# Optimization experiments

Measured on AMD Instinct MI355X. Metric: run time of the kernel, lower is better.

The kernel has to match this reference:

```python
import jax, jax.numpy as jnp
import numpy as np

N, E, IN, HID, OUT = 50000, 800000, 256, 256, 64
HEADS, DH = 4, 64  # GAT: hidden//4 per head, concat=False -> mean over heads
EPS = 1e-5


def _gcn(x, W, b, src, dst):
    # PyG GCNConv: h = xW; add self-loops; sym-normalized scatter-add; + bias
    n = x.shape[0]
    h = x @ W
    deg = jnp.zeros((n,), x.dtype).at[dst].add(1.0) + 1.0  # +1 for self-loop
    dinv = jax.lax.rsqrt(deg)
    norm = dinv[src] * dinv[dst]                      # [E]
    out = jax.ops.segment_sum(h[src] * norm[:, None], dst, num_segments=n)
    out = out + h * (dinv * dinv)[:, None]            # self-loop term
    return out + b


def _gat(x, W, a_s, a_d, b, src, dst):
    # PyG GATConv(heads=HEADS, concat=False): per-edge attention softmax over
    # incoming edges (incl. self-loop), LeakyReLU(0.2) logits, mean over heads.
    n = x.shape[0]
    h = (x @ W).reshape(n, HEADS, DH)
    al_s = jnp.einsum('nhd,hd->nh', h, a_s)           # [N,H]
    al_d = jnp.einsum('nhd,hd->nh', h, a_d)
    e = jax.nn.leaky_relu(al_s[src] + al_d[dst], 0.2)  # [E,H]
    e_self = jax.nn.leaky_relu(al_s + al_d, 0.2)       # [N,H]
    m = jnp.maximum(jax.ops.segment_max(e, dst, num_segments=n), e_self)
    ee = jnp.exp(e - m[dst])
    es = jnp.exp(e_self - m)
    denom = jax.ops.segment_sum(ee, dst, num_segments=n) + es        # [N,H]
    numer = jax.ops.segment_sum(ee[:, :, None] * h[src], dst, num_segments=n) + es[:, :, None] * h
    return (numer / denom[:, :, None]).mean(axis=1) + b


def _bn(x, g, b):
    # BatchNorm1d over node dim, batch statistics (training-mode math)
    mu = x.mean(axis=0)
    var = x.var(axis=0)
    return g * (x - mu) * jax.lax.rsqrt(var + EPS) + b


def setup_inputs() -> dict:
    key = jax.random.key(0)
    ks = jax.random.split(key, 12)
    s = lambda d: 1.0 / np.sqrt(d)
    inp = {
        'x': jax.random.normal(ks[0], (N, IN), jnp.float32),
        'edge_index': jax.random.randint(ks[1], (2, E), 0, N, jnp.int64),
        'W1': jax.random.normal(ks[2], (IN, HID), jnp.float32) * s(IN),
        'b1': jnp.zeros((HID,), jnp.float32),
        'g1': jnp.ones((HID,), jnp.float32),
        'be1': jnp.zeros((HID,), jnp.float32),
        'Wg': jax.random.normal(ks[3], (HID, HEADS * DH), jnp.float32) * s(HID),
        'a_src': jax.random.normal(ks[4], (HEADS, DH), jnp.float32) * s(DH),
        'a_dst': jax.random.normal(ks[5], (HEADS, DH), jnp.float32) * s(DH),
        'bg': jnp.zeros((DH,), jnp.float32),
        'g2': jnp.ones((DH,), jnp.float32),
        'be2': jnp.zeros((DH,), jnp.float32),
        'W3': jax.random.normal(ks[6], (64, 16), jnp.float32) * s(64),
        'b3': jnp.zeros((16,), jnp.float32),
        'g3': jnp.ones((16,), jnp.float32),
        'be3': jnp.zeros((16,), jnp.float32),
        'W4': jax.random.normal(ks[7], (16, OUT), jnp.float32) * s(16),
        'b4': jnp.zeros((OUT,), jnp.float32),
        'r1W': jax.random.normal(ks[8], (IN, HID), jnp.float32) * s(IN),
        'r1b': jnp.zeros((HID,), jnp.float32),
        'r2W': jax.random.normal(ks[9], (HID, 64), jnp.float32) * s(HID),
        'r2b': jnp.zeros((64,), jnp.float32),
        'r3W': jax.random.normal(ks[10], (64, 16), jnp.float32) * s(64),
        'r3b': jnp.zeros((16,), jnp.float32),
        'pW': jax.random.normal(ks[11], (OUT, OUT), jnp.float32) * s(OUT),
        'pb': jnp.zeros((OUT,), jnp.float32),
    }
    return inp


def reference(x, edge_index, W1, b1, g1, be1, Wg, a_src, a_dst, bg, g2, be2,
              W3, b3, g3, be3, W4, b4, r1W, r1b, r2W, r2b, r3W, r3b, pW, pb):
    src, dst = edge_index[0], edge_index[1]
    slope = 0.01  # F.leaky_relu default; dropout is identity at inference
    x0 = x
    h = _gcn(x0, W1, b1, src, dst)
    h = jax.nn.leaky_relu(_bn(h, g1, be1), slope)
    h = h + (x0 @ r1W + r1b)
    x2 = h
    h = _gat(x2, Wg, a_src, a_dst, bg, src, dst)
    h = jax.nn.leaky_relu(_bn(h, g2, be2), slope)
    h = h + (x2 @ r2W + r2b)
    x3 = h
    h = _gcn(x3, W3, b3, src, dst)
    h = jax.nn.leaky_relu(_bn(h, g3, be3), slope)
    h = h + (x3 @ r3W + r3b)
    h = _gcn(h, W4, b4, src, dst)
    return h @ pW + pb
```

## Files before the change

kernel.cpp:

```cpp
#include <hip/hip_runtime.h>

typedef unsigned short u16;
typedef unsigned int   u32;

__device__ __forceinline__ float b2f(u16 h){ return __uint_as_float(((u32)h)<<16); }
__device__ __forceinline__ u16 f2b(float f){
  u32 u = __float_as_uint(f);
  u32 r = (u + 0x7fffu + ((u>>16)&1u)) >> 16;
  return (u16)r;
}
__device__ __forceinline__ float leaky(float x, float s){ return x >= 0.f ? x : s*x; }

typedef __bf16 bf16x8 __attribute__((ext_vector_type(8)));
typedef float  f32x4  __attribute__((ext_vector_type(4)));

__device__ __forceinline__ float ldval(const u16* p){ return b2f(*p); }
__device__ __forceinline__ float ldval(const float* p){ return *p; }

__device__ __forceinline__ void load8(const u16* p, u16* h){ *(uint4*)h = *(const uint4*)p; }
__device__ __forceinline__ void load8(const float* p, u16* h){
  float4 a = *(const float4*)p; float4 b = *(const float4*)(p+4);
  h[0]=f2b(a.x); h[1]=f2b(a.y); h[2]=f2b(a.z); h[3]=f2b(a.w);
  h[4]=f2b(b.x); h[5]=f2b(b.y); h[6]=f2b(b.z); h[7]=f2b(b.w);
}

__global__ void k_detect(const u32* __restrict__ w, int E, u32* __restrict__ flag){
  u32 acc = 0;
  for (int i = blockIdx.x*256 + threadIdx.x; i < E; i += 256*gridDim.x)
    acc |= w[2*i + 1];
  __shared__ u32 s[256];
  s[threadIdx.x] = acc; __syncthreads();
  for (int o=128;o>0;o>>=1){ if (threadIdx.x<o) s[threadIdx.x] |= s[threadIdx.x+o]; __syncthreads(); }
  if (threadIdx.x==0 && s[0]) atomicOr(flag, 1u);
}

__device__ __forceinline__ void edge_sd(const int* __restrict__ ei, int E, int e, u32 is32,
                                        int& s, int& d){
  if (is32){ s = ei[e];   d = ei[E + e]; }
  else     { s = ei[2*e]; d = ei[2*E + 2*e]; }
}

__global__ void k_hist(const int* __restrict__ ei, int E, int nN,
                       const u32* __restrict__ flag, int* __restrict__ cnt){
  int e = blockIdx.x*256 + threadIdx.x;
  if (e < E){
    int s,d; edge_sd(ei, E, e, *flag, s, d);
    if ((u32)s < (u32)nN && (u32)d < (u32)nN) atomicAdd(&cnt[d], 1);
  }
}

__global__ void k_scan_a(const int* __restrict__ cnt, int n, int* __restrict__ bsum){
  __shared__ int s[256];
  int base = blockIdx.x*1024, t = threadIdx.x, sum = 0;
  for (int j=0;j<4;j++){ int i = base + t*4 + j; if (i<n) sum += cnt[i]; }
  s[t] = sum; __syncthreads();
  for (int off=128; off>0; off>>=1){ if (t<off) s[t]+=s[t+off]; __syncthreads(); }
  if (t==0) bsum[blockIdx.x] = s[0];
}

__global__ void k_scan_b(int* bsum, int nb){
  if (threadIdx.x==0 && blockIdx.x==0){
    int acc = 0;
    for (int i=0;i<nb;i++){ int v = bsum[i]; bsum[i] = acc; acc += v; }
  }
}

__global__ void k_scan_c(const int* __restrict__ cnt, const int* __restrict__ bsum,
                         int n, int* __restrict__ offs){
  __shared__ int s[256];
  int base = blockIdx.x*1024, t = threadIdx.x;
  int v[4]; int sum=0;
  for (int j=0;j<4;j++){ int i=base+t*4+j; v[j] = (i<n)?cnt[i]:0; sum += v[j]; }
  s[t]=sum; __syncthreads();
  for (int off=1; off<256; off<<=1){
    int add = (t>=off)? s[t-off] : 0;
    __syncthreads();
    s[t] += add;
    __syncthreads();
  }
  int excl = (t ? s[t-1] : 0) + bsum[blockIdx.x];
  for (int j=0;j<4;j++){
    int i = base+t*4+j;
    if (i<n){ offs[i] = excl; excl += v[j]; if (i==n-1) offs[n] = excl; }
  }
}

__global__ void k_dinv2(const int* __restrict__ offs, int n, float* __restrict__ dinv){
  int i = blockIdx.x*256+threadIdx.x;
  if (i<n) dinv[i] = rsqrtf((float)(offs[i+1]-offs[i]) + 1.0f);
}

__global__ void k_scatter(const int* __restrict__ ei, int E, int nN,
                          const u32* __restrict__ flag, const int* __restrict__ offs,
                          int* __restrict__ cursor, int* __restrict__ csr){
  int e = blockIdx.x*256+threadIdx.x;
  if (e<E){
    int s,d; edge_sd(ei, E, e, *flag, s, d);
    if ((u32)s < (u32)nN && (u32)d < (u32)nN){
      int pos = offs[d] + atomicAdd(&cursor[d], 1);
      csr[pos] = s;
    }
  }
}

__global__ void k_transpose(const float* __restrict__ in, u16* __restrict__ out, int K, int M){
  int i = blockIdx.x*256 + threadIdx.x;
  if (i < K*M){ int k = i / M, m = i % M; out[m*K + k] = f2b(in[i]); }
}

__global__ void k_asdt(const float* __restrict__ a_s, const float* __restrict__ a_d,
                       float* __restrict__ asi, float* __restrict__ adi){
  int i = threadIdx.x;
  int h = i>>6, c = i&63;
  asi[c*4+h] = a_s[i];
  adi[c*4+h] = a_d[i];
}

template<typename AT>
__global__ __launch_bounds__(256) void k_gemm64(
  const AT* __restrict__ A0, const AT* __restrict__ A1,
  const AT* __restrict__ A2, const AT* __restrict__ A3,
  int rsA, const u16* __restrict__ Bt, const float* __restrict__ bias,
  u16* __restrict__ out, int nRows)
{
  alignas(16) __shared__ u16 Al[64*264];
  const int t = threadIdx.x;
  const int r0 = blockIdx.x*64;
  for (int it=0; it<8; ++it){
    int c = t + it*256;
    int row = c>>5, seg = c&31;
    int gr = r0+row;
    u16 hv[8] = {0,0,0,0,0,0,0,0};
    if (gr < nRows){
      const AT* p = (seg<8)?A0 : (seg<16)?A1 : (seg<24)?A2 : A3;
      load8(p + (size_t)gr*rsA + (seg&7)*8, hv);
    }
    *(uint4*)&Al[row*264 + seg*8] = *(uint4*)hv;
  }
  const int lane=t&63, wid=t>>6, quad=lane>>4, l15=lane&15;
  __syncthreads();
  const int col = wid*16 + l15;
  const u16* Bp = Bt + (size_t)col*256 + quad*8;
  bf16x8 b[8];
  #pragma unroll
  for (int ks=0;ks<8;++ks) b[ks] = *(const bf16x8*)(Bp + ks*32);
  f32x4 acc[4] = {{0.f,0.f,0.f,0.f},{0.f,0.f,0.f,0.f},{0.f,0.f,0.f,0.f},{0.f,0.f,0.f,0.f}};
  #pragma unroll
  for (int rt=0; rt<4; ++rt){
    const int abase = (rt*16 + l15)*264 + quad*8;
    #pragma unroll
    for (int ks=0;ks<8;++ks){
      bf16x8 av = *(const bf16x8*)&Al[abase + ks*32];
      acc[rt] = __builtin_amdgcn_mfma_f32_16x16x32_bf16(av, b[ks], acc[rt], 0,0,0);
    }
  }
  __syncthreads();
  float bv = bias ? bias[col] : 0.f;
  #pragma unroll
  for (int rt=0; rt<4; ++rt){
    #pragma unroll
    for (int reg=0;reg<4;++reg)
      Al[(rt*16 + quad*4 + reg)*264 + col] = f2b(acc[rt][reg]+bv);
  }
  __syncthreads();
  #pragma unroll
  for (int it=0; it<2; ++it){
    int idx = it*256 + t;
    int row = idx>>3, cu = idx&7;
    if (r0+row < nRows)
      *(uint4*)(out + (size_t)(r0+row)*64 + cu*8) = *(const uint4*)&Al[row*264 + cu*8];
  }
}

template<typename AT, bool PERM, bool EW, bool DOT, bool RS>
__global__ __launch_bounds__(512) void k_gemm256(
  const AT* __restrict__ A0, const AT* __restrict__ A1,
  const AT* __restrict__ A2, const AT* __restrict__ A3,
  int rsA, const u16* __restrict__ Bt, const float* __restrict__ bias,
  const u16* __restrict__ agg, const float* __restrict__ bnp,
  const float* __restrict__ asi, const float* __restrict__ adi,
  float* __restrict__ als, float* __restrict__ ald,
  const float* __restrict__ rowscale,
  u16* __restrict__ out, int nRows)
{
  alignas(16) __shared__ u16 Al[64*264];
  const int t = threadIdx.x;
  const int r0 = blockIdx.x*64;
  for (int it=0; it<4; ++it){
    int c = t + it*512;
    int row = c>>5, seg = c&31;
    int gr = r0+row;
    u16 hv[8] = {0,0,0,0,0,0,0,0};
    if (gr < nRows){
      const AT* p = (seg<8)?A0 : (seg<16)?A1 : (seg<24)?A2 : A3;
      load8(p + (size_t)gr*rsA + (seg&7)*8, hv);
    }
    *(uint4*)&Al[row*264 + seg*8] = *(uint4*)hv;
  }
  const int lane=t&63, wid=t>>6, quad=lane>>4, l15=lane&15;
  __syncthreads();
  f32x4 acc[2][4];
  #pragma unroll
  for (int ct=0; ct<2; ++ct)
    #pragma unroll
    for (int rt=0; rt<4; ++rt) acc[ct][rt] = {0.f,0.f,0.f,0.f};
  #pragma unroll
  for (int ct=0; ct<2; ++ct){
    const u16* Bp = Bt + (size_t)(wid*32 + ct*16 + l15)*256 + quad*8;
    #pragma unroll
    for (int ks=0;ks<8;++ks){
      bf16x8 b = *(const bf16x8*)(Bp + ks*32);
      #pragma unroll
      for (int rt=0; rt<4; ++rt){
        bf16x8 av = *(const bf16x8*)&Al[(rt*16 + l15)*264 + quad*8 + ks*32];
        acc[ct][rt] = __builtin_amdgcn_mfma_f32_16x16x32_bf16(av, b, acc[ct][rt], 0,0,0);
      }
    }
  }
  __syncthreads();
  #pragma unroll
  for (int ct=0; ct<2; ++ct){
    int col = wid*32 + ct*16 + l15;
    float bv = bias ? bias[col] : 0.f;
    int oc = PERM ? ((col&63)*4 + (col>>6)) : col;
    #pragma unroll
    for (int rt=0; rt<4; ++rt){
      #pragma unroll
      for (int reg=0;reg<4;++reg){
        float v = acc[ct][rt][reg] + bv;
        if constexpr (RS){
          int r = r0 + rt*16 + quad*4 + reg;
          v *= (r < nRows) ? rowscale[r] : 1.f;
        }
        Al[(rt*16 + quad*4 + reg)*264 + oc] = f2b(v);
      }
    }
  }
  __syncthreads();
  if constexpr (DOT){
    int row = t>>3, q = t&7;
    int nd = r0 + row;
    if (nd < nRows){
      float s0=0.f,s1=0.f,s2=0.f,s3=0.f,d0=0.f,d1=0.f,d2=0.f,d3=0.f;
      const u16* ar = &Al[row*264 + q*32];
      const float* as = asi + q*32;
      const float* ad = adi + q*32;
      #pragma unroll 4
      for (int k=0;k<32;k+=4){
        uint2 wv = *(const uint2*)&ar[k];
        float v0=b2f((u16)(wv.x&0xffff)), v1=b2f((u16)(wv.x>>16));
        float v2=b2f((u16)(wv.y&0xffff)), v3=b2f((u16)(wv.y>>16));
        s0 += v0*as[k];   d0 += v0*ad[k];
        s1 += v1*as[k+1]; d1 += v1*ad[k+1];
        s2 += v2*as[k+2]; d2 += v2*ad[k+2];
        s3 += v3*as[k+3]; d3 += v3*ad[k+3];
      }
      s0 += __shfl_xor(s0,1,64); s0 += __shfl_xor(s0,2,64); s0 += __shfl_xor(s0,4,64);
      s1 += __shfl_xor(s1,1,64); s1 += __shfl_xor(s1,2,64); s1 += __shfl_xor(s1,4,64);
      s2 += __shfl_xor(s2,1,64); s2 += __shfl_xor(s2,2,64); s2 += __shfl_xor(s2,4,64);
      s3 += __shfl_xor(s3,1,64); s3 += __shfl_xor(s3,2,64); s3 += __shfl_xor(s3,4,64);
      d0 += __shfl_xor(d0,1,64); d0 += __shfl_xor(d0,2,64); d0 += __shfl_xor(d0,4,64);
      d1 += __shfl_xor(d1,1,64); d1 += __shfl_xor(d1,2,64); d1 += __shfl_xor(d1,4,64);
      d2 += __shfl_xor(d2,1,64); d2 += __shfl_xor(d2,2,64); d2 += __shfl_xor(d2,4,64);
      d3 += __shfl_xor(d3,1,64); d3 += __shfl_xor(d3,2,64); d3 += __shfl_xor(d3,4,64);
      if (q==0){
        float4 sv = {s0,s1,s2,s3}; float4 dv = {d0,d1,d2,d3};
        ((float4*)als)[nd] = sv;
        ((float4*)ald)[nd] = dv;
      }
    }
  }
  #pragma unroll
  for (int it=0; it<4; ++it){
    int idx = it*512 + t;
    int row = idx>>5, cu = idx&31;
    int r = r0+row;
    if (r < nRows){
      if constexpr (EW){
        uint4 hv = *(const uint4*)&Al[row*264 + cu*8];
        uint4 av = *(const uint4*)(agg + (size_t)r*256 + cu*8);
        const u16* hp = (const u16*)&hv; const u16* ap = (const u16*)&av;
        uint4 ov; u16* op = (u16*)&ov;
        #pragma unroll
        for (int j=0;j<8;++j){
          int c = cu*8+j;
          float v = b2f(ap[j])*bnp[c] + bnp[256+c];
          op[j] = f2b(leaky(v, 0.01f) + b2f(hp[j]));
        }
        *(uint4*)(out + (size_t)r*256 + cu*8) = ov;
      } else {
        *(uint4*)(out + (size_t)r*256 + cu*8) = *(const uint4*)&Al[row*264 + cu*8];
      }
    }
  }
}

__global__ void k_gather64(const u16* __restrict__ h, const int* __restrict__ offs,
                           const int* __restrict__ csr, const float* __restrict__ dinv,
                           const float* __restrict__ bias, int n, u16* __restrict__ out){
  int nd = blockIdx.x*4 + (threadIdx.x>>6);
  if (nd>=n) return;
  int lane = threadIdx.x&63;
  float dn = dinv[nd];
  float acc = dn*b2f(h[(size_t)nd*64+lane]);
  int e = offs[nd], end = offs[nd+1];
  for (; e+4<=end; e+=4){
    int s0=csr[e], s1=csr[e+1], s2=csr[e+2], s3=csr[e+3];
    float w0=dinv[s0], w1=dinv[s1], w2=dinv[s2], w3=dinv[s3];
    float p0=b2f(h[(size_t)s0*64+lane]);
    float p1=b2f(h[(size_t)s1*64+lane]);
    float p2=b2f(h[(size_t)s2*64+lane]);
    float p3=b2f(h[(size_t)s3*64+lane]);
    acc += w0*p0 + w1*p1 + w2*p2 + w3*p3;
  }
  for (; e<end; ++e){
    int s=csr[e];
    acc += dinv[s]*b2f(h[(size_t)s*64+lane]);
  }
  out[(size_t)nd*64+lane] = f2b(dn*acc + bias[lane]);
}

__global__ void k_gather256(const u16* __restrict__ h, const int* __restrict__ offs,
                            const int* __restrict__ csr, const float* __restrict__ dinv,
                            const float* __restrict__ bias, int n, u16* __restrict__ out){
  int nd = blockIdx.x*4 + (threadIdx.x>>6);
  if (nd>=n) return;
  int lane = threadIdx.x&63;
  const uint2* H = (const uint2*)h;
  float dn = dinv[nd];
  uint2 pv = H[(size_t)nd*64 + lane];
  float a0=b2f(pv.x&0xffff), a1=b2f(pv.x>>16);
  float a2=b2f(pv.y&0xffff), a3=b2f(pv.y>>16);
  int e=offs[nd], end=offs[nd+1];
  for (; e+4<=end; e+=4){
    int s0=csr[e], s1=csr[e+1], s2=csr[e+2], s3=csr[e+3];
    uint2 q0=H[(size_t)s0*64+lane], q1=H[(size_t)s1*64+lane];
    uint2 q2=H[(size_t)s2*64+lane], q3=H[(size_t)s3*64+lane];
    a0 += b2f(q0.x&0xffff) + b2f(q1.x&0xffff) + b2f(q2.x&0xffff) + b2f(q3.x&0xffff);
    a1 += b2f(q0.x>>16)    + b2f(q1.x>>16)    + b2f(q2.x>>16)    + b2f(q3.x>>16);
    a2 += b2f(q0.y&0xffff) + b2f(q1.y&0xffff) + b2f(q2.y&0xffff) + b2f(q3.y&0xffff);
    a3 += b2f(q0.y>>16)    + b2f(q1.y>>16)    + b2f(q2.y>>16)    + b2f(q3.y>>16);
  }
  for (; e<end; ++e){
    int s=csr[e];
    uint2 q=H[(size_t)s*64+lane];
    a0 += b2f(q.x&0xffff); a1 += b2f(q.x>>16);
    a2 += b2f(q.y&0xffff); a3 += b2f(q.y>>16);
  }
  float4 bv = *(const float4*)(bias + lane*4);
  uint2 o;
  o.x = (u32)f2b(a0*dn + bv.x) | ((u32)f2b(a1*dn + bv.y)<<16);
  o.y = (u32)f2b(a2*dn + bv.z) | ((u32)f2b(a3*dn + bv.w)<<16);
  ((uint2*)out)[(size_t)nd*64 + lane] = o;
}

template<typename T, int C>
__global__ __launch_bounds__(256) void k_stats_part(const T* __restrict__ x, int n,
                                                    float* __restrict__ part){
  constexpr int VE = 16/sizeof(T);
  constexpr int G  = C/VE;
  constexpr int R  = 256/G;
  int t = threadIdx.x;
  int g = t % G, sub = t / G;
  int rpb = (n + gridDim.x - 1) / gridDim.x;
  int base = blockIdx.x * rpb;
  int lim  = min(base + rpb, n);
  float s[VE], s2[VE];
  #pragma unroll
  for (int j=0;j<VE;j++){ s[j]=0.f; s2[j]=0.f; }
  #pragma unroll 4
  for (int r = base + sub; r < lim; r += R){
    const T* p = x + (size_t)r*C + g*VE;
    if constexpr (sizeof(T)==2){
      uint4 v = *(const uint4*)p;
      u32 wq[4] = {v.x, v.y, v.z, v.w};
      #pragma unroll
      for (int q=0;q<4;q++){
        float lo = __uint_as_float(wq[q]<<16);
        float hi = __uint_as_float(wq[q]&0xffff0000u);
        s[2*q]  += lo; s2[2*q]  += lo*lo;
        s[2*q+1]+= hi; s2[2*q+1]+= hi*hi;
      }
    } else {
      float4 v = *(const float4*)p;
      float a[4] = {v.x, v.y, v.z, v.w};
      #pragma unroll
      for (int q=0;q<4;q++){ s[q]+=a[q]; s2[q]+=a[q]*a[q]; }
    }
  }
  __shared__ float red[VE][256];
  #pragma unroll
  for (int j=0;j<VE;j++) red[j][t] = s[j];
  __syncthreads();
  for (int off=R/2; off>0; off>>=1){
    if (sub < off){
      #pragma unroll
      for (int j=0;j<VE;j++) red[j][t] += red[j][t + off*G];
    }
    __syncthreads();
  }
  if (t < G){
    #pragma unroll
    for (int j=0;j<VE;j++) part[blockIdx.x*2*C + t*VE + j] = red[j][t];
  }
  __syncthreads();
  #pragma unroll
  for (int j=0;j<VE;j++) red[j][t] = s2[j];
  __syncthreads();
  for (int off=R/2; off>0; off>>=1){
    if (sub < off){
      #pragma unroll
      for (int j=0;j<VE;j++) red[j][t] += red[j][t + off*G];
    }
    __syncthreads();
  }
  if (t < G){
    #pragma unroll
    for (int j=0;j<VE;j++) part[blockIdx.x*2*C + C + t*VE + j] = red[j][t];
  }
}

template<int C>
__global__ __launch_bounds__(256) void k_bnfin3(const float* __restrict__ part, int B,
                         const float* __restrict__ g, const float* __restrict__ be,
                         float n, float* __restrict__ bnp){
  constexpr int CPB = (C < 32) ? C : 32;
  constexpr int TPC = 256 / CPB;
  int t = threadIdx.x;
  int lc = t % CPB, sub = t / CPB;
  int c = blockIdx.x*CPB + lc;
  float s=0.f, s2=0.f;
  for (int b = sub; b < B; b += TPC){
    s  += part[(size_t)b*2*C + c];
    s2 += part[(size_t)b*2*C + C + c];
  }
  __shared__ float ls[256], lq[256];
  ls[t]=s; lq[t]=s2; __syncthreads();
  for (int off=TPC/2; off>0; off>>=1){
    if (sub < off){ ls[t]+=ls[t+off*CPB]; lq[t]+=lq[t+off*CPB]; }
    __syncthreads();
  }
  if (sub==0){
    float mu = ls[t]/n;
    float var = fmaxf(lq[t]/n - mu*mu, 0.f);
    float sc = g[c] * rsqrtf(var + 1e-5f);
    bnp[c] = sc;
    bnp[C+c] = be[c] - mu*sc;
  }
}

__global__ void k_ew_b16b16(const u16* __restrict__ agg, const u16* __restrict__ res,
                            const float* __restrict__ bnp, int C, int total, u16* __restrict__ out){
  int i = blockIdx.x*256+threadIdx.x;
  if (i < total){
    int c = i & (C-1);
    float v = b2f(agg[i])*bnp[c] + bnp[C+c];
    out[i] = f2b(leaky(v, 0.01f) + b2f(res[i]));
  }
}

__global__ void k_ew_f32f32(const float* __restrict__ agg, const float* __restrict__ res,
                            const float* __restrict__ bnp, int C, int total, float* __restrict__ out){
  int i = blockIdx.x*256+threadIdx.x;
  if (i < total){
    int c = i & (C-1);
    float v = agg[i]*bnp[c] + bnp[C+c];
    out[i] = leaky(v, 0.01f) + res[i];
  }
}

__global__ void k_dot64(const u16* __restrict__ h2t, const float* __restrict__ asg,
                        const float* __restrict__ adg, int head, int n,
                        float* __restrict__ als, float* __restrict__ ald){
  int nd = blockIdx.x*4 + (threadIdx.x>>6);
  if (nd>=n) return;
  int lane = threadIdx.x&63;
  float p = b2f(h2t[(size_t)nd*64+lane]);
  float ss = p*asg[lane];
  float sd = p*adg[lane];
  for (int m=1;m<64;m<<=1){ ss += __shfl_xor(ss,m,64); sd += __shfl_xor(sd,m,64); }
  if (lane==0){ als[nd*4+head]=ss; ald[nd*4+head]=sd; }
}

__global__ void k_gat_head(const u16* __restrict__ h2t, const int* __restrict__ offs,
                           const int* __restrict__ csr, const float* __restrict__ als,
                           const float* __restrict__ ald, const float* __restrict__ bg,
                           int head, int n, u16* __restrict__ O2){
  int nd = blockIdx.x*4 + (threadIdx.x>>6);
  if (nd>=n) return;
  int lane = threadIdx.x&63;
  float aldn = ald[nd*4+head];
  float m = leaky(als[nd*4+head] + aldn, 0.2f);
  float denom = 1.f;
  float acc = b2f(h2t[(size_t)nd*64+lane]);
  int e = offs[nd], end = offs[nd+1];
  for (; e+4<=end; e+=4){
    int s0=csr[e], s1=csr[e+1], s2=csr[e+2], s3=csr[e+3];
    float l0=als[s0*4+head], l1=als[s1*4+head], l2=als[s2*4+head], l3=als[s3*4+head];
    float p0=b2f(h2t[(size_t)s0*64+lane]);
    float p1=b2f(h2t[(size_t)s1*64+lane]);
    float p2=b2f(h2t[(size_t)s2*64+lane]);
    float p3=b2f(h2t[(size_t)s3*64+lane]);
    float g0=leaky(l0+aldn,0.2f), g1=leaky(l1+aldn,0.2f);
    float g2=leaky(l2+aldn,0.2f), g3=leaky(l3+aldn,0.2f);
    float mc = fmaxf(fmaxf(g0,g1), fmaxf(g2,g3));
    float mn = fmaxf(m, mc);
    float sc = __expf(m - mn);
    float w0 = __expf(g0-mn), w1 = __expf(g1-mn), w2 = __expf(g2-mn), w3 = __expf(g3-mn);
    denom = denom*sc + (w0+w1+w2+w3);
    acc   = acc*sc   + (w0*p0 + w1*p1 + w2*p2 + w3*p3);
    m = mn;
  }
  for (; e<end; ++e){
    int s = csr[e];
    float g = leaky(als[s*4+head]+aldn, 0.2f);
    float p = b2f(h2t[(size_t)s*64+lane]);
    float mn = fmaxf(m, g);
    float sc = __expf(m - mn);
    float w = __expf(g - mn);
    denom = denom*sc + w;
    acc   = acc*sc   + w*p;
    m = mn;
  }
  float v = 0.25f * acc / fmaxf(denom, 1e-20f);
  size_t oi = (size_t)nd*64+lane;
  if (head==0) O2[oi] = f2b(v + bg[lane]);
  else         O2[oi] = f2b(b2f(O2[oi]) + v);
}

__global__ void k_gat_all(const u16* __restrict__ h2i, const int* __restrict__ offs,
                          const int* __restrict__ csr, const float* __restrict__ als,
                          const float* __restrict__ ald, const float* __restrict__ bg,
                          int n, u16* __restrict__ O2){
  alignas(16) __shared__ float shm[4][80];
  int wv = threadIdx.x>>6;
  int nd = blockIdx.x*4 + wv;
  if (nd>=n) return;
  int lane = threadIdx.x&63;
  int eg = lane>>2, hh = lane&3;
  float4 alv = ((const float4*)als)[nd];
  float4 adv = ((const float4*)ald)[nd];
  float adh = (hh&2) ? ((hh&1)?adv.w:adv.z) : ((hh&1)?adv.y:adv.x);
  float alh = (hh&2) ? ((hh&1)?alv.w:alv.z) : ((hh&1)?alv.y:alv.x);
  float gsh = leaky(alh+adh, 0.2f);
  int beg=offs[nd], end=offs[nd+1];
  float m = gsh;
  for (int e=beg+eg; e<end; e+=16){
    int s = csr[e];
    m = fmaxf(m, leaky(als[s*4+hh]+adh, 0.2f));
  }
  #pragma unroll
  for (int off=4; off<64; off<<=1) m = fmaxf(m, __shfl_xor(m, off, 64));
  float wsh = __expf(gsh - m);
  if (eg==0) shm[wv][4+hh] = wsh;
  float4 ws4 = *(const float4*)&shm[wv][4];
  uint2 pv = ((const uint2*)h2i)[(size_t)nd*64+lane];
  float a0 = ws4.x*__uint_as_float(pv.x<<16);
  float a1 = ws4.y*__uint_as_float(pv.x&0xffff0000u);
  float a2 = ws4.z*__uint_as_float(pv.y<<16);
  float a3 = ws4.w*__uint_as_float(pv.y&0xffff0000u);
  float dpart = 0.f;
  const uint2* H = (const uint2*)h2i;
  for (int e0=beg; e0<end; e0+=16){
    int e = e0+eg;
    int sA = 0; float wE = 0.f;
    if (e<end){
      sA = csr[e];
      wE = __expf(leaky(als[sA*4+hh]+adh, 0.2f) - m);
    }
    dpart += wE;
    shm[wv][8+lane] = wE;
    int cnt = min(16, end-e0);
    int k=0;
    for (; k+4<=cnt; k+=4){
      int sa=__shfl(sA,(k  )*4,64), sb=__shfl(sA,(k+1)*4,64);
      int sc=__shfl(sA,(k+2)*4,64), sd=__shfl(sA,(k+3)*4,64);
      float4 wa=*(const float4*)&shm[wv][8+(k  )*4];
      float4 wb=*(const float4*)&shm[wv][8+(k+1)*4];
      float4 wc=*(const float4*)&shm[wv][8+(k+2)*4];
      float4 wd=*(const float4*)&shm[wv][8+(k+3)*4];
      uint2 qa=H[(size_t)sa*64+lane], qb=H[(size_t)sb*64+lane];
      uint2 qc=H[(size_t)sc*64+lane], qd=H[(size_t)sd*64+lane];
      a0 += wa.x*__uint_as_float(qa.x<<16) + wb.x*__uint_as_float(qb.x<<16)
          + wc.x*__uint_as_float(qc.x<<16) + wd.x*__uint_as_float(qd.x<<16);
      a1 += wa.y*__uint_as_float(qa.x&0xffff0000u) + wb.y*__uint_as_float(qb.x&0xffff0000u)
          + wc.y*__uint_as_float(qc.x&0xffff0000u) + wd.y*__uint_as_float(qd.x&0xffff0000u);
      a2 += wa.z*__uint_as_float(qa.y<<16) + wb.z*__uint_as_float(qb.y<<16)
          + wc.z*__uint_as_float(qc.y<<16) + wd.z*__uint_as_float(qd.y<<16);
      a3 += wa.w*__uint_as_float(qa.y&0xffff0000u) + wb.w*__uint_as_float(qb.y&0xffff0000u)
          + wc.w*__uint_as_float(qc.y&0xffff0000u) + wd.w*__uint_as_float(qd.y&0xffff0000u);
    }
    for (; k<cnt; ++k){
      int s = __shfl(sA, k*4, 64);
      float4 w4 = *(const float4*)&shm[wv][8+k*4];
      uint2 q = H[(size_t)s*64+lane];
      a0 += w4.x*__uint_as_float(q.x<<16);
      a1 += w4.y*__uint_as_float(q.x&0xffff0000u);
      a2 += w4.z*__uint_as_float(q.y<<16);
      a3 += w4.w*__uint_as_float(q.y&0xffff0000u);
    }
  }
  #pragma unroll
  for (int off=4; off<64; off<<=1) dpart += __shfl_xor(dpart, off, 64);
  float dh = dpart + wsh;
  if (eg==0) shm[wv][hh] = dh;
  float4 d4 = *(const float4*)&shm[wv][0];
  float v = 0.25f*(a0/d4.x + a1/d4.y + a2/d4.z + a3/d4.w);
  O2[(size_t)nd*64+lane] = f2b(v + bg[lane]);
}

__global__ void k_gcn_agg16(const float* __restrict__ h, const int* __restrict__ offs,
                            const int* __restrict__ csr, const float* __restrict__ dinv,
                            const float* __restrict__ bias, float* __restrict__ out, int n){
  int t = threadIdx.x;
  int nd = blockIdx.x*16 + (t>>4);
  if (nd>=n) return;
  int c = t&15;
  float dn = dinv[nd];
  float acc = h[(size_t)nd*16+c];
  int e=offs[nd], end=offs[nd+1];
  for (; e+4<=end; e+=4){
    int s0=csr[e], s1=csr[e+1], s2=csr[e+2], s3=csr[e+3];
    acc += h[(size_t)s0*16+c] + h[(size_t)s1*16+c]
         + h[(size_t)s2*16+c] + h[(size_t)s3*16+c];
  }
  for (; e<end; ++e){
    int s = csr[e];
    acc += h[(size_t)s*16+c];
  }
  out[(size_t)nd*16+c] = dn*acc + bias[c];
}

__global__ void k_gcn_agg64f(const float* __restrict__ h, const int* __restrict__ offs,
                             const int* __restrict__ csr, const float* __restrict__ dinv,
                             const float* __restrict__ bias, float* __restrict__ out, int n){
  int nd = blockIdx.x*4 + (threadIdx.x>>6);
  if (nd>=n) return;
  int lane = threadIdx.x&63;
  float dn = dinv[nd];
  float acc = h[(size_t)nd*64+lane];
  int e=offs[nd], end=offs[nd+1];
  for (; e+4<=end; e+=4){
    int s0=csr[e], s1=csr[e+1], s2=csr[e+2], s3=csr[e+3];
    acc += h[(size_t)s0*64+lane] + h[(size_t)s1*64+lane]
         + h[(size_t)s2*64+lane] + h[(size_t)s3*64+lane];
  }
  for (; e<end; ++e){
    int s=csr[e];
    acc += h[(size_t)s*64+lane];
  }
  out[(size_t)nd*64+lane] = dn*acc + bias[lane];
}

__global__ void k_gemm64_16x2(const u16* __restrict__ x, const float* __restrict__ W1_,
                              const float* __restrict__ W2_, const float* __restrict__ b2_,
                              const float* __restrict__ dinv,
                              int n, float* __restrict__ o1, float* __restrict__ o2){
  __shared__ float w1[64*16], w2[64*16];
  int t = threadIdx.x;
  for (int i=t; i<1024; i+=256){ w1[i]=W1_[i]; w2[i]=W2_[i]; }
  __syncthreads();
  int nd = blockIdx.x*8 + (t>>5);
  if (nd>=n) return;
  int j = t & 31;
  const u16* xr = x + (size_t)nd*64;
  if (j<16){
    float s=0.f;
    #pragma unroll 8
    for (int k=0;k<64;k++) s += b2f(xr[k])*w1[k*16+j];
    o1[(size_t)nd*16+j]=s*dinv[nd];
  } else {
    int jj=j-16;
    float s = b2_[jj];
    #pragma unroll 8
    for (int k=0;k<64;k++) s += b2f(xr[k])*w2[k*16+jj];
    o2[(size_t)nd*16+jj]=s;
  }
}

__global__ void k_gemm16_64(const float* __restrict__ x, const float* __restrict__ W,
                            const float* __restrict__ dinv,
                            int n, float* __restrict__ o){
  __shared__ float w[16*64];
  int t = threadIdx.x;
  for (int i=t;i<1024;i+=256) w[i]=W[i];
  __syncthreads();
  int nd = blockIdx.x*4 + (t>>6);
  if (nd>=n) return;
  int j = t&63;
  const float* xr = x + (size_t)nd*16;
  float s=0.f;
  #pragma unroll
  for (int k=0;k<16;k++) s += xr[k]*w[k*64+j];
  o[(size_t)nd*64+j]=s*dinv[nd];
}

__global__ void k_final(const float* __restrict__ x, const float* __restrict__ W,
                        const float* __restrict__ b, int n, float* __restrict__ out){
  __shared__ float w[64*64];
  int t=threadIdx.x;
  for (int i=t;i<4096;i+=256) w[i]=W[i];
  __syncthreads();
  int nd = blockIdx.x*4 + (t>>6);
  if (nd>=n) return;
  int j=t&63;
  const float* xr = x + (size_t)nd*64;
  float s=b[j];
  #pragma unroll 8
  for (int k=0;k<64;k++) s += xr[k]*w[k*64+j];
  out[(size_t)nd*64+j]=s;
}

extern "C" void kernel_launch(void* const* d_in, const int* in_sizes, int n_in,
                              void* d_out, int out_size, void* d_ws, size_t ws_size,
                              hipStream_t stream) {
  const float* x   = (const float*)d_in[0];
  const int*   ei  = (const int*)d_in[1];
  const float* W1  = (const float*)d_in[2];
  const float* b1  = (const float*)d_in[3];
  const float* g1  = (const float*)d_in[4];
  const float* be1 = (const float*)d_in[5];
  const float* Wg  = (const float*)d_in[6];
  const float* a_s = (const float*)d_in[7];
  const float* a_d = (const float*)d_in[8];
  const float* bg  = (const float*)d_in[9];
  const float* g2  = (const float*)d_in[10];
  const float* be2 = (const float*)d_in[11];
  const float* W3  = (const float*)d_in[12];
  const float* b3  = (const float*)d_in[13];
  const float* g3  = (const float*)d_in[14];
  const float* be3 = (const float*)d_in[15];
  const float* W4  = (const float*)d_in[16];
  const float* b4  = (const float*)d_in[17];
  const float* r1W = (const float*)d_in[18];
  const float* r1b = (const float*)d_in[19];
  const float* r2W = (const float*)d_in[20];
  const float* r2b = (const float*)d_in[21];
  const float* r3W = (const float*)d_in[22];
  const float* r3b = (const float*)d_in[23];
  const float* pW  = (const float*)d_in[24];
  const float* pb  = (const float*)d_in[25];

  const int N = in_sizes[0] / 256;
  const int E = in_sizes[1] / 2;

  char* w = (char*)d_ws;
  auto alloc = [&](size_t b)->void*{ void* p=(void*)w; w += (b+255)&~(size_t)255; return p; };
  u32*   flag   = (u32*)  alloc(4);
  float* part   = (float*)alloc(256*512*4);
  float* bnp1   = (float*)alloc(512*4);
  float* bnp2   = (float*)alloc(128*4);
  float* bnp3   = (float*)alloc(32*4);
  int*   bsum   = (int*)  alloc(256*4);
  int*   cur    = (int*)  alloc((size_t)N*4);
  int*   offs   = (int*)  alloc((size_t)(N+1)*4);
  float* dinv   = (float*)alloc((size_t)N*4);
  int*   csr    = (int*)  alloc((size_t)E*4);
  float* als    = (float*)alloc((size_t)N*16);
  float* ald    = (float*)alloc((size_t)N*16);
  float* asi    = (float*)alloc(256*4);
  float* adi    = (float*)alloc(256*4);
  u16*   W1t    = (u16*)  alloc(65536*2);
  u16*   r1Wt   = (u16*)  alloc(65536*2);
  u16*   Wgt    = (u16*)  alloc(65536*2);
  u16*   r2Wt   = (u16*)  alloc(16384*2);

  auto cdiv = [](int a, int b){ return (a+b-1)/b; };
  const int nb1024 = cdiv(N, 1024);
  const int statsGrid = 256;
  const int gemmGrid = cdiv(N,64);
  const int nodeGrid = cdiv(N,4);

  hipMemsetAsync(flag,   0, 4, stream);
  hipMemsetAsync(cur,    0, (size_t)N*4, stream);

  k_detect<<<64,256,0,stream>>>((const u32*)ei, E, flag);

  k_transpose<<<cdiv(65536,256),256,0,stream>>>(W1,  W1t,  256,256);
  k_transpose<<<cdiv(65536,256),256,0,stream>>>(r1W, r1Wt, 256,256);
  k_transpose<<<cdiv(65536,256),256,0,stream>>>(Wg,  Wgt,  256,256);
  k_transpose<<<cdiv(16384,256),256,0,stream>>>(r2W, r2Wt, 256,64);
  k_asdt<<<1,256,0,stream>>>(a_s, a_d, asi, adi);

  k_hist  <<<cdiv(E,256),256,0,stream>>>(ei, E, N, flag, cur);
  k_scan_a<<<nb1024,256,0,stream>>>(cur, N, bsum);
  k_scan_b<<<1,64,0,stream>>>(bsum, nb1024);
  k_scan_c<<<nb1024,256,0,stream>>>(cur, bsum, N, offs);
  k_dinv2 <<<cdiv(N,256),256,0,stream>>>(offs, N, dinv);
  hipMemsetAsync(cur, 0, (size_t)N*4, stream);
  k_scatter<<<cdiv(E,256),256,0,stream>>>(ei, E, N, flag, offs, cur, csr);

  size_t miscUsed = (size_t)(w - (char*)d_ws);
  size_t bigNeed  = miscUsed + 2*((size_t)N*512) + 1024;

  if (ws_size >= bigNeed){
    u16* RA = (u16*)alloc((size_t)N*512);
    u16* RB = (u16*)alloc((size_t)N*512);
    u16* tAe = (u16*)d_in[1];
    u16* r2d = (u16*)d_out;

    float* h3   = (float*)RA;
    float* r3   = (float*)(RA + (size_t)N*32);
    float* agg3 = (float*)(RA + (size_t)N*64);
    float* x4   = (float*)(RA + (size_t)N*96);
    float* h4   = (float*)RB;
    float* agg4 = (float*)d_out;

    k_gemm256<float,false,false,false,true><<<gemmGrid,512,0,stream>>>(
        x, x+64, x+128, x+192, 256, W1t, nullptr,
        nullptr, nullptr, nullptr, nullptr, nullptr, nullptr, dinv, RA, N);
    k_gather256<<<nodeGrid,256,0,stream>>>(RA, offs, csr, dinv, b1, N, RB);
    k_stats_part<u16,256><<<statsGrid,256,0,stream>>>(RB, N, part);
    k_bnfin3<256><<<8,256,0,stream>>>(part, statsGrid, g1, be1, (float)N, bnp1);
    k_gemm256<float,false,true,false,false><<<gemmGrid,512,0,stream>>>(
        x, x+64, x+128, x+192, 256, r1Wt, r1b,
        RB, bnp1, nullptr, nullptr, nullptr, nullptr, nullptr, RB, N);

    k_gemm256<u16,true,false,true,false><<<gemmGrid,512,0,stream>>>(
        RB, RB+64, RB+128, RB+192, 256, Wgt, nullptr,
        nullptr, nullptr, asi, adi, als, ald, nullptr, RA, N);
    k_gemm64<u16><<<gemmGrid,256,0,stream>>>(RB, RB+64, RB+128, RB+192, 256,
                                             r2Wt, r2b, r2d, N);
    k_gat_all<<<nodeGrid,256,0,stream>>>(RA, offs, csr, als, ald, bg, N, tAe);
    k_stats_part<u16,64><<<statsGrid,256,0,stream>>>(tAe, N, part);
    k_bnfin3<64><<<2,256,0,stream>>>(part, statsGrid, g2, be2, (float)N, bnp2);
    k_ew_b16b16<<<cdiv(N*64,256),256,0,stream>>>(tAe, r2d, bnp2, 64, N*64, tAe);

    k_gemm64_16x2<<<cdiv(N,8),256,0,stream>>>(tAe, W3, r3W, r3b, dinv, N, h3, r3);
    k_gcn_agg16<<<cdiv(N,16),256,0,stream>>>(h3, offs, csr, dinv, b3, agg3, N);
    k_stats_part<float,16><<<statsGrid,256,0,stream>>>(agg3, N, part);
    k_bnfin3<16><<<1,256,0,stream>>>(part, statsGrid, g3, be3, (float)N, bnp3);
    k_ew_f32f32<<<cdiv(N*16,256),256,0,stream>>>(agg3, r3, bnp3, 16, N*16, x4);

    k_gemm16_64<<<nodeGrid,256,0,stream>>>(x4, W4, dinv, N, h4);
    k_gcn_agg64f<<<nodeGrid,256,0,stream>>>(h4, offs, csr, dinv, b4, agg4, N);
    k_final<<<nodeGrid,256,0,stream>>>(agg4, pW, pb, N, (float*)d_out);
  } else {
    u16* X0 = (u16*)alloc((size_t)N*64*2);
    u16* X1 = (u16*)alloc((size_t)N*64*2);
    u16* tA = (u16*)alloc((size_t)N*64*2);
    u16* tB = (u16*)alloc((size_t)N*64*2);
    u16* X2 = (u16*)d_in[1];
    u16* X3 = (u16*)d_out;
    const u16* XP[4] = {X0, X1, X2, X3};

    float* h3   = (float*)X1;
    float* r3   = (float*)(X1 + (size_t)N*32);
    float* agg3 = (float*)tA;
    float* x4   = (float*)(tA + (size_t)N*32);
    float* h4   = (float*)X0;
    float* agg4 = (float*)tA;

    for (int tau=0; tau<4; ++tau){
      u16* Xt = (u16*)XP[tau];
      k_gemm64<float><<<gemmGrid,256,0,stream>>>(x, x+64, x+128, x+192, 256,
                                                 W1t + (size_t)tau*64*256, nullptr, tA, N);
      k_gather64<<<nodeGrid,256,0,stream>>>(tA, offs, csr, dinv, b1 + tau*64, N, tB);
      k_stats_part<u16,64><<<statsGrid,256,0,stream>>>(tB, N, part);
      k_bnfin3<64><<<2,256,0,stream>>>(part, statsGrid, g1 + tau*64, be1 + tau*64, (float)N, bnp1 + tau*128);
      k_gemm64<float><<<gemmGrid,256,0,stream>>>(x, x+64, x+128, x+192, 256,
                                                 r1Wt + (size_t)tau*64*256, r1b + tau*64, tA, N);
      k_ew_b16b16<<<cdiv(N*64,256),256,0,stream>>>(tB, tA, bnp1 + tau*128, 64, N*64, Xt);
    }

    for (int head=0; head<4; ++head){
      k_gemm64<u16><<<gemmGrid,256,0,stream>>>(XP[0], XP[1], XP[2], XP[3], 64,
                                               Wgt + (size_t)head*64*256, nullptr, tA, N);
      k_dot64<<<nodeGrid,256,0,stream>>>(tA, a_s + head*64, a_d + head*64, head, N, als, ald);
      k_gat_head<<<nodeGrid,256,0,stream>>>(tA, offs, csr, als, ald, bg, head, N, tB);
    }
    k_gemm64<u16><<<gemmGrid,256,0,stream>>>(XP[0], XP[1], XP[2], XP[3], 64,
                                             r2Wt, r2b, tA, N);
    k_stats_part<u16,64><<<statsGrid,256,0,stream>>>(tB, N, part);
    k_bnfin3<64><<<2,256,0,stream>>>(part, statsGrid, g2, be2, (float)N, bnp2);
    k_ew_b16b16<<<cdiv(N*64,256),256,0,stream>>>(tB, tA, bnp2, 64, N*64, X0);

    k_gemm64_16x2<<<cdiv(N,8),256,0,stream>>>(X0, W3, r3W, r3b, dinv, N, h3, r3);
    k_gcn_agg16<<<cdiv(N,16),256,0,stream>>>(h3, offs, csr, dinv, b3, agg3, N);
    k_stats_part<float,16><<<statsGrid,256,0,stream>>>(agg3, N, part);
    k_bnfin3<16><<<1,256,0,stream>>>(part, statsGrid, g3, be3, (float)N, bnp3);
    k_ew_f32f32<<<cdiv(N*16,256),256,0,stream>>>(agg3, r3, bnp3, 16, N*16, x4);

    k_gemm16_64<<<nodeGrid,256,0,stream>>>(x4, W4, dinv, N, h4);
    k_gcn_agg64f<<<nodeGrid,256,0,stream>>>(h4, offs, csr, dinv, b4, agg4, N);
    k_final<<<nodeGrid,256,0,stream>>>(agg4, pW, pb, N, (float*)d_out);
  }
}
```

Before: 700.9 us.

## Merge prep kernels, fold dinv into scan, add nontemporal CSR loads

Folds the four weight-transpose launches and the attention-vector reshuffle into one k_prep launch, and computes dinv inside the scan kernel from the per-node counts, removing k_dinv2. CSR index reads in the gather and aggregation kernels become nontemporal loads, and some outputs use nontemporal stores, so streaming data is less likely to evict reused feature rows from cache. The 256-wide gather is unrolled to 8 edges per iteration for more loads in flight, at the cost of extra registers. Launch savings are small, and the cache hints may do little.

```diff
diff --git a/kernel.cpp b/kernel.cpp
--- a/kernel.cpp
+++ b/kernel.cpp
@@ -2,6 +2,7 @@
 
 typedef unsigned short u16;
 typedef unsigned int   u32;
+typedef unsigned long long u64;
 
 __device__ __forceinline__ float b2f(u16 h){ return __uint_as_float(((u32)h)<<16); }
 __device__ __forceinline__ u16 f2b(float f){
@@ -66,7 +67,7 @@
 }
 
 __global__ void k_scan_c(const int* __restrict__ cnt, const int* __restrict__ bsum,
-                         int n, int* __restrict__ offs){
+                         int n, int* __restrict__ offs, float* __restrict__ dinv){
   __shared__ int s[256];
   int base = blockIdx.x*1024, t = threadIdx.x;
   int v[4]; int sum=0;
@@ -81,13 +82,12 @@
   int excl = (t ? s[t-1] : 0) + bsum[blockIdx.x];
   for (int j=0;j<4;j++){
     int i = base+t*4+j;
-    if (i<n){ offs[i] = excl; excl += v[j]; if (i==n-1) offs[n] = excl; }
-  }
-}
-
-__global__ void k_dinv2(const int* __restrict__ offs, int n, float* __restrict__ dinv){
-  int i = blockIdx.x*256+threadIdx.x;
-  if (i<n) dinv[i] = rsqrtf((float)(offs[i+1]-offs[i]) + 1.0f);
+    if (i<n){
+      offs[i] = excl; excl += v[j];
+      dinv[i] = rsqrtf((float)v[j] + 1.0f);
+      if (i==n-1) offs[n] = excl;
+    }
+  }
 }
 
 __global__ void k_scatter(const int* __restrict__ ei, int E, int nN,
@@ -103,17 +103,18 @@
   }
 }
 
-__global__ void k_transpose(const float* __restrict__ in, u16* __restrict__ out, int K, int M){
-  int i = blockIdx.x*256 + threadIdx.x;
-  if (i < K*M){ int k = i / M, m = i % M; out[m*K + k] = f2b(in[i]); }
-}
-
-__global__ void k_asdt(const float* __restrict__ a_s, const float* __restrict__ a_d,
+__global__ void k_prep(const float* __restrict__ W1, const float* __restrict__ r1W,
+                       const float* __restrict__ Wg, const float* __restrict__ r2W,
+                       const float* __restrict__ a_s, const float* __restrict__ a_d,
+                       u16* __restrict__ W1t, u16* __restrict__ r1Wt,
+                       u16* __restrict__ Wgt, u16* __restrict__ r2Wt,
                        float* __restrict__ asi, float* __restrict__ adi){
-  int i = threadIdx.x;
-  int h = i>>6, c = i&63;
-  asi[c*4+h] = a_s[i];
-  adi[c*4+h] = a_d[i];
+  int b = blockIdx.x, t = threadIdx.x;
+  if (b < 256){        int i=b*256+t;        int k=i>>8, m=i&255; W1t [m*256+k]=f2b(W1 [i]); }
+  else if (b < 512){   int i=(b-256)*256+t;  int k=i>>8, m=i&255; r1Wt[m*256+k]=f2b(r1W[i]); }
+  else if (b < 768){   int i=(b-512)*256+t;  int k=i>>8, m=i&255; Wgt [m*256+k]=f2b(Wg [i]); }
+  else if (b < 832){   int i=(b-768)*256+t;  int k=i>>6, m=i&63;  r2Wt[m*256+k]=f2b(r2W[i]); }
+  else {               int h=t>>6, c=t&63;   asi[c*4+h]=a_s[t];   adi[c*4+h]=a_d[t]; }
 }
 
 template<typename AT>
@@ -305,7 +306,10 @@
   float acc = dn*b2f(h[(size_t)nd*64+lane]);
   int e = offs[nd], end = offs[nd+1];
   for (; e+4<=end; e+=4){
-    int s0=csr[e], s1=csr[e+1], s2=csr[e+2], s3=csr[e+3];
+    int s0=__builtin_nontemporal_load(&csr[e]);
+    int s1=__builtin_nontemporal_load(&csr[e+1]);
+    int s2=__builtin_nontemporal_load(&csr[e+2]);
+    int s3=__builtin_nontemporal_load(&csr[e+3]);
     float w0=dinv[s0], w1=dinv[s1], w2=dinv[s2], w3=dinv[s3];
     float p0=b2f(h[(size_t)s0*64+lane]);
     float p1=b2f(h[(size_t)s1*64+lane]);
@@ -332,14 +336,27 @@
   float a0=b2f(pv.x&0xffff), a1=b2f(pv.x>>16);
   float a2=b2f(pv.y&0xffff), a3=b2f(pv.y>>16);
   int e=offs[nd], end=offs[nd+1];
-  for (; e+4<=end; e+=4){
-    int s0=csr[e], s1=csr[e+1], s2=csr[e+2], s3=csr[e+3];
+  for (; e+8<=end; e+=8){
+    int s0=__builtin_nontemporal_load(&csr[e  ]);
+    int s1=__builtin_nontemporal_load(&csr[e+1]);
+    int s2=__builtin_nontemporal_load(&csr[e+2]);
+    int s3=__builtin_nontemporal_load(&csr[e+3]);
+    int s4=__builtin_nontemporal_load(&csr[e+4]);
+    int s5=__builtin_nontemporal_load(&csr[e+5]);
+    int s6=__builtin_nontemporal_load(&csr[e+6]);
+    int s7=__builtin_nontemporal_load(&csr[e+7]);
     uint2 q0=H[(size_t)s0*64+lane], q1=H[(size_t)s1*64+lane];
     uint2 q2=H[(size_t)s2*64+lane], q3=H[(size_t)s3*64+lane];
-    a0 += b2f(q0.x&0xffff) + b2f(q1.x&0xffff) + b2f(q2.x&0xffff) + b2f(q3.x&0xffff);
-    a1 += b2f(q0.x>>16)    + b2f(q1.x>>16)    + b2f(q2.x>>16)    + b2f(q3.x>>16);
-    a2 += b2f(q0.y&0xffff) + b2f(q1.y&0xffff) + b2f(q2.y&0xffff) + b2f(q3.y&0xffff);
-    a3 += b2f(q0.y>>16)    + b2f(q1.y>>16)    + b2f(q2.y>>16)    + b2f(q3.y>>16);
+    uint2 q4=H[(size_t)s4*64+lane], q5=H[(size_t)s5*64+lane];
+    uint2 q6=H[(size_t)s6*64+lane], q7=H[(size_t)s7*64+lane];
+    a0 += b2f(q0.x&0xffff) + b2f(q1.x&0xffff) + b2f(q2.x&0xffff) + b2f(q3.x&0xffff)
+        + b2f(q4.x&0xffff) + b2f(q5.x&0xffff) + b2f(q6.x&0xffff) + b2f(q7.x&0xffff);
+    a1 += b2f(q0.x>>16)    + b2f(q1.x>>16)    + b2f(q2.x>>16)    + b2f(q3.x>>16)
+        + b2f(q4.x>>16)    + b2f(q5.x>>16)    + b2f(q6.x>>16)    + b2f(q7.x>>16);
+    a2 += b2f(q0.y&0xffff) + b2f(q1.y&0xffff) + b2f(q2.y&0xffff) + b2f(q3.y&0xffff)
+        + b2f(q4.y&0xffff) + b2f(q5.y&0xffff) + b2f(q6.y&0xffff) + b2f(q7.y&0xffff);
+    a3 += b2f(q0.y>>16)    + b2f(q1.y>>16)    + b2f(q2.y>>16)    + b2f(q3.y>>16)
+        + b2f(q4.y>>16)    + b2f(q5.y>>16)    + b2f(q6.y>>16)    + b2f(q7.y>>16);
   }
   for (; e<end; ++e){
     int s=csr[e];
@@ -348,10 +365,10 @@
     a2 += b2f(q.y&0xffff); a3 += b2f(q.y>>16);
   }
   float4 bv = *(const float4*)(bias + lane*4);
-  uint2 o;
-  o.x = (u32)f2b(a0*dn + bv.x) | ((u32)f2b(a1*dn + bv.y)<<16);
-  o.y = (u32)f2b(a2*dn + bv.z) | ((u32)f2b(a3*dn + bv.w)<<16);
-  ((uint2*)out)[(size_t)nd*64 + lane] = o;
+  u32 lo = (u32)f2b(a0*dn + bv.x) | ((u32)f2b(a1*dn + bv.y)<<16);
+  u32 hi = (u32)f2b(a2*dn + bv.z) | ((u32)f2b(a3*dn + bv.w)<<16);
+  u64 packed = (u64)lo | ((u64)hi<<32);
+  __builtin_nontemporal_store(packed, (u64*)(out + (size_t)nd*256 + lane*4));
 }
 
 template<typename T, int C>
@@ -546,7 +563,7 @@
   int beg=offs[nd], end=offs[nd+1];
   float m = gsh;
   for (int e=beg+eg; e<end; e+=16){
-    int s = csr[e];
+    int s = __builtin_nontemporal_load(&csr[e]);
     m = fmaxf(m, leaky(als[s*4+hh]+adh, 0.2f));
   }
   #pragma unroll
@@ -565,7 +582,7 @@
     int e = e0+eg;
     int sA = 0; float wE = 0.f;
     if (e<end){
-      sA = csr[e];
+      sA = __builtin_nontemporal_load(&csr[e]);
       wE = __expf(leaky(als[sA*4+hh]+adh, 0.2f) - m);
     }
     dpart += wE;
@@ -606,7 +623,7 @@
   if (eg==0) shm[wv][hh] = dh;
   float4 d4 = *(const float4*)&shm[wv][0];
   float v = 0.25f*(a0/d4.x + a1/d4.y + a2/d4.z + a3/d4.w);
-  O2[(size_t)nd*64+lane] = f2b(v + bg[lane]);
+  __builtin_nontemporal_store((u16)f2b(v + bg[lane]), &O2[(size_t)nd*64+lane]);
 }
 
 __global__ void k_gcn_agg16(const float* __restrict__ h, const int* __restrict__ offs,
@@ -620,7 +637,10 @@
   float acc = h[(size_t)nd*16+c];
   int e=offs[nd], end=offs[nd+1];
   for (; e+4<=end; e+=4){
-    int s0=csr[e], s1=csr[e+1], s2=csr[e+2], s3=csr[e+3];
+    int s0=__builtin_nontemporal_load(&csr[e]);
+    int s1=__builtin_nontemporal_load(&csr[e+1]);
+    int s2=__builtin_nontemporal_load(&csr[e+2]);
+    int s3=__builtin_nontemporal_load(&csr[e+3]);
     acc += h[(size_t)s0*16+c] + h[(size_t)s1*16+c]
          + h[(size_t)s2*16+c] + h[(size_t)s3*16+c];
   }
@@ -641,7 +661,10 @@
   float acc = h[(size_t)nd*64+lane];
   int e=offs[nd], end=offs[nd+1];
   for (; e+4<=end; e+=4){
-    int s0=csr[e], s1=csr[e+1], s2=csr[e+2], s3=csr[e+3];
+    int s0=__builtin_nontemporal_load(&csr[e]);
+    int s1=__builtin_nontemporal_load(&csr[e+1]);
+    int s2=__builtin_nontemporal_load(&csr[e+2]);
+    int s3=__builtin_nontemporal_load(&csr[e+3]);
     acc += h[(size_t)s0*64+lane] + h[(size_t)s1*64+lane]
          + h[(size_t)s2*64+lane] + h[(size_t)s3*64+lane];
   }
@@ -775,18 +798,12 @@
   hipMemsetAsync(cur,    0, (size_t)N*4, stream);
 
   k_detect<<<64,256,0,stream>>>((const u32*)ei, E, flag);
-
-  k_transpose<<<cdiv(65536,256),256,0,stream>>>(W1,  W1t,  256,256);
-  k_transpose<<<cdiv(65536,256),256,0,stream>>>(r1W, r1Wt, 256,256);
-  k_transpose<<<cdiv(65536,256),256,0,stream>>>(Wg,  Wgt,  256,256);
-  k_transpose<<<cdiv(16384,256),256,0,stream>>>(r2W, r2Wt, 256,64);
-  k_asdt<<<1,256,0,stream>>>(a_s, a_d, asi, adi);
+  k_prep<<<833,256,0,stream>>>(W1, r1W, Wg, r2W, a_s, a_d, W1t, r1Wt, Wgt, r2Wt, asi, adi);
 
   k_hist  <<<cdiv(E,256),256,0,stream>>>(ei, E, N, flag, cur);
   k_scan_a<<<nb1024,256,0,stream>>>(cur, N, bsum);
   k_scan_b<<<1,64,0,stream>>>(bsum, nb1024);
-  k_scan_c<<<nb1024,256,0,stream>>>(cur, bsum, N, offs);
-  k_dinv2 <<<cdiv(N,256),256,0,stream>>>(offs, N, dinv);
+  k_scan_c<<<nb1024,256,0,stream>>>(cur, bsum, N, offs, dinv);
   hipMemsetAsync(cur, 0, (size_t)N*4, stream);
   k_scatter<<<cdiv(E,256),256,0,stream>>>(ei, E, N, flag, offs, cur, csr);
 
```

New measurement: 703.1 us. No clear change (+0.3%).
